# Kernel optimization log

Measured on AMD Instinct MI355X. Metric: run time of the kernel, lower is better.

The kernel has to match this reference:

```python
import jax, jax.numpy as jnp
import numpy as np

B, S, E, H = 4, 1024, 1024, 16
HD = E // H
MAX_SEQ = 5000


def setup_inputs() -> dict:
    key = jax.random.key(0)
    ks = jax.random.split(key, 10)
    def lin(kw, kb):
        w = jax.random.normal(kw, (E, E), dtype=jnp.float32) * (1.0 / np.sqrt(E))
        b = jax.random.normal(kb, (E,), dtype=jnp.float32) * 0.01
        return w, b
    wq, bq = lin(ks[0], ks[1])
    wk, bk = lin(ks[2], ks[3])
    wv, bv = lin(ks[4], ks[5])
    wo, bo = lin(ks[6], ks[7])
    rpe_table = jax.random.normal(ks[8], (H, 2 * MAX_SEQ - 1, HD), dtype=jnp.float32) * 0.02
    x = jax.random.normal(ks[9], (B, S, E), dtype=jnp.float32)
    return {"x": x, "wq": wq, "bq": bq, "wk": wk, "bk": bk,
            "wv": wv, "bv": bv, "wo": wo, "bo": bo, "rpe_table": rpe_table}


def reference(x, wq, bq, wk, bk, wv, bv, wo, bo, rpe_table):
    b, s, e = x.shape
    scale = 1.0 / np.sqrt(HD)
    # projections (torch Linear: y = x @ W^T + b), reshape to (b, h, s, hd)
    q = (x @ wq.T + bq).reshape(b, s, H, HD).transpose(0, 2, 1, 3)
    k = (x @ wk.T + bk).reshape(b, s, H, HD).transpose(0, 2, 1, 3)
    v = (x @ wv.T + bv).reshape(b, s, H, HD).transpose(0, 2, 1, 3)
    scores = jnp.einsum('bhqd,bhkd->bhqk', q, k) * scale
    # RPE: rpe[h, q, k, d] = table[h, q - k + s - 1, d]; factor the einsum:
    # rel[b,h,q,r] = sum_d q[b,h,q,d] * table[h,r,d], then gather r = q - k + s - 1
    table = rpe_table[:, : 2 * s - 1]               # (H, 2s-1, HD)
    rel = jnp.einsum('bhqd,hrd->bhqr', q, table)    # (b, H, s, 2s-1)
    idx = jnp.arange(s)[:, None] - jnp.arange(s)[None, :] + (s - 1)  # (s, s)
    rpe_scores = jnp.take_along_axis(
        rel, jnp.broadcast_to(idx[None, None], (b, H, s, s)), axis=-1)
    attn = jax.nn.softmax(scores + rpe_scores, axis=-1)
    ctx = jnp.einsum('bhqk,bhkd->bhqd', attn, v)
    ctx = ctx.transpose(0, 2, 1, 3).reshape(b, s, e)
    return ctx @ wo.T + bo
```

## Files before the change

### kernel.cpp

```cpp
#include <hip/hip_runtime.h>
#include <hip/hip_bf16.h>
#include <stdint.h>

typedef __attribute__((ext_vector_type(8))) short s8v;
typedef __attribute__((ext_vector_type(4))) float f32x4;
typedef __attribute__((ext_vector_type(16))) float f32x16;

union V16 { uint4 u4; unsigned int u[4]; s8v s; };

__device__ inline s8v u4_to_s8(uint4 v) { V16 c; c.u4 = v; return c.s; }
__device__ inline s8v words_to_s8(unsigned int a, unsigned int b, unsigned int c, unsigned int d) {
  V16 t; t.u[0] = a; t.u[1] = b; t.u[2] = c; t.u[3] = d; return t.s;
}
__device__ inline unsigned short f2b(float f) {
  __hip_bfloat16 h = __float2bfloat16(f);
  unsigned short u; __builtin_memcpy(&u, &h, 2); return u;
}
__device__ inline unsigned int pack2(float lo, float hi) {
  return ((unsigned int)f2b(hi) << 16) | (unsigned int)f2b(lo);
}
__device__ inline unsigned int cvtpk(float lo, float hi) {
  unsigned int r; asm("v_cvt_pk_bf16_f32 %0, %1, %2" : "=v"(r) : "v"(lo), "v"(hi)); return r;
}
__device__ inline float exp2_fast(float x) {
#if __has_builtin(__builtin_amdgcn_exp2f)
  return __builtin_amdgcn_exp2f(x);
#else
  float y; asm("v_exp_f32 %0, %1" : "=v"(y) : "v"(x)); return y;
#endif
}
__device__ inline void gld16(const void* g, void* lds) {
  __builtin_amdgcn_global_load_lds((const __attribute__((address_space(1))) void*)g,
                                   (__attribute__((address_space(3))) void*)lds, 16, 0, 0);
}

#define LOG2E 1.4426950408889634f

__global__ void cvt_all_kernel(const float* __restrict__ x, const float* __restrict__ wq,
                               const float* __restrict__ wk, const float* __restrict__ wv,
                               const float* __restrict__ wo,
                               __hip_bfloat16* __restrict__ XB, __hip_bfloat16* __restrict__ WQKV,
                               __hip_bfloat16* __restrict__ WOb) {
  size_t i = ((size_t)blockIdx.x * 256 + threadIdx.x) * 8;
  const float* src; __hip_bfloat16* dst; size_t off;
  if (i < 4194304)      { src = x;  dst = XB;             off = i; }
  else if (i < 5242880) { src = wq; dst = WQKV;           off = i - 4194304; }
  else if (i < 6291456) { src = wk; dst = WQKV + 1048576; off = i - 5242880; }
  else if (i < 7340032) { src = wv; dst = WQKV + 2097152; off = i - 6291456; }
  else                  { src = wo; dst = WOb;            off = i - 7340032; }
  const float4* s4 = (const float4*)(src + off);
  float4 a = s4[0], b = s4[1];
  uint4 o;
  o.x = pack2(a.x, a.y); o.y = pack2(a.z, a.w);
  o.z = pack2(b.x, b.y); o.w = pack2(b.z, b.w);
  *(uint4*)(dst + off) = o;
}

__global__ void cvt_tbl_kernel(const float* __restrict__ tb, __hip_bfloat16* __restrict__ TBL) {
  size_t i = ((size_t)blockIdx.x * 256 + threadIdx.x) * 8;
  int h = (int)(i >> 17);
  int rem = (int)(i & 131071);
  int r = rem >> 6, c = rem & 63;
  uint4 o;
  if (r < 2047) {
    const float4* s4 = (const float4*)(tb + ((size_t)h * 9999 + r) * 64 + c);
    float4 a = s4[0], b = s4[1];
    o.x = pack2(a.x * LOG2E, a.y * LOG2E); o.y = pack2(a.z * LOG2E, a.w * LOG2E);
    o.z = pack2(b.x * LOG2E, b.y * LOG2E); o.w = pack2(b.z * LOG2E, b.w * LOG2E);
  } else { o.x = 0u; o.y = 0u; o.z = 0u; o.w = 0u; }
  *(uint4*)(TBL + i) = o;
}

template<int MODE>
__global__ __launch_bounds__(256, 3) void gemm_bt(
    const __hip_bfloat16* __restrict__ A,
    const __hip_bfloat16* __restrict__ Bt,
    const float* __restrict__ bias0,
    const float* __restrict__ bias1,
    void* __restrict__ out0,
    void* __restrict__ out1) {
  __shared__ __align__(16) char smem[32768];
  char* As = smem;
  char* Bs = smem + 16384;
  const int tid = threadIdx.x;
  const int w = tid >> 6, l = tid & 63;
  const int wr = w >> 1, wc = w & 1;
  const int lr = l & 15, lg = l >> 4;
  const int m0 = blockIdx.y * 128, n0 = blockIdx.x * 128;

  f32x4 acc[4][4] = {};

  for (int kt = 0; kt < 16; ++kt) {
    __syncthreads();
    #pragma unroll
    for (int i = 0; i < 4; ++i) {
      const int off = i * 4096 + w * 1024;
      const int loff = off + l * 16;
      const int row = loff >> 7;
      const int cb = loff & 127;
      const int sc = cb ^ ((row & 7) << 4);
      gld16((const char*)A  + (size_t)(m0 + row) * 2048 + kt * 128 + sc, As + off);
      gld16((const char*)Bt + (size_t)(n0 + row) * 2048 + kt * 128 + sc, Bs + off);
    }
    asm volatile("s_waitcnt vmcnt(0)" ::: "memory");
    __syncthreads();
    #pragma unroll
    for (int ks = 0; ks < 2; ++ks) {
      uint4 af[4], bf4[4];
      #pragma unroll
      for (int i = 0; i < 4; ++i) {
        const int ra = wr * 64 + i * 16 + lr;
        const int rb = wc * 64 + i * 16 + lr;
        const int cb = ks * 64 + lg * 16;
        af[i]  = *(const uint4*)(As + ra * 128 + (cb ^ ((ra & 7) << 4)));
        bf4[i] = *(const uint4*)(Bs + rb * 128 + (cb ^ ((rb & 7) << 4)));
      }
      #pragma unroll
      for (int i = 0; i < 4; ++i) {
        #pragma unroll
        for (int j = 0; j < 4; ++j)
          acc[i][j] = __builtin_amdgcn_mfma_f32_16x16x32_bf16(u4_to_s8(af[i]), u4_to_s8(bf4[j]), acc[i][j], 0, 0, 0);
      }
    }
  }

  const int mrow = m0 + wr * 64 + lg * 4;
  const int ncol = n0 + wc * 64 + lr;

  if constexpr (MODE == 0) {
    const float KSCALE = 0.125f * LOG2E;
    #pragma unroll
    for (int j = 0; j < 4; ++j) {
      const int n = ncol + j * 16;
      const bool isQ = n < 1024;
      __hip_bfloat16* op = isQ ? (__hip_bfloat16*)out0 : (__hip_bfloat16*)out1;
      const int nn = isQ ? n : n - 1024;
      const float bia = isQ ? bias0[n] : bias1[n - 1024];
      const float sc = isQ ? 1.0f : KSCALE;
      const int hh = nn >> 6, hd = nn & 63;
      #pragma unroll
      for (int i = 0; i < 4; ++i) {
        #pragma unroll
        for (int r = 0; r < 4; ++r) {
          const int m = mrow + i * 16 + r;
          const int bb = m >> 10, ss = m & 1023;
          op[(((size_t)(bb * 16 + hh)) * 1024 + ss) * 64 + hd] = __float2bfloat16((acc[i][j][r] + bia) * sc);
        }
      }
    }
  } else if constexpr (MODE == 1) {
    #pragma unroll
    for (int i = 0; i < 4; ++i) {
      #pragma unroll
      for (int r = 0; r < 4; ++r) {
        const int f = mrow + i * 16 + r;
        const float bia = bias0[f];
        const int fh = f >> 6, fd = f & 63;
        #pragma unroll
        for (int j = 0; j < 4; ++j) {
          const int bs = ncol + j * 16;
          const int bb = bs >> 10, ss = bs & 1023;
          ((__hip_bfloat16*)out0)[(size_t)bb * 1048576 + (size_t)fh * 65536 + fd * 1024 + ss] =
              __float2bfloat16(acc[i][j][r] + bia);
        }
      }
    }
  } else {
    #pragma unroll
    for (int j = 0; j < 4; ++j) {
      const int n = ncol + j * 16;
      const float bia = bias0[n];
      #pragma unroll
      for (int i = 0; i < 4; ++i) {
        #pragma unroll
        for (int r = 0; r < 4; ++r) {
          const int m = mrow + i * 16 + r;
          ((float*)out0)[(size_t)m * 1024 + n] = acc[i][j][r] + bia;
        }
      }
    }
  }
}

__global__ __launch_bounds__(256, 2) void attn_kernel(
    const __hip_bfloat16* __restrict__ Qg,
    const __hip_bfloat16* __restrict__ Kg,
    const __hip_bfloat16* __restrict__ VTg,
    const __hip_bfloat16* __restrict__ Tg,
    __hip_bfloat16* __restrict__ Cg) {
  __shared__ __align__(16) char smem[73984];
  char* Klds = smem;
  char* Vlds = smem + 8192;
  char* Tlds = smem + 16384;
  const int tid = threadIdx.x;
  const int w = tid >> 6, l = tid & 63;
  const int ql = l & 31, half = l >> 5;
  char* relw = smem + 40960 + w * 8192;
  char* dumpp = smem + 73728 + l * 4;

  const int bx = blockIdx.x;
  const int qt = bx & 7, h = (bx >> 3) & 15, b = bx >> 7;
  const int qb = qt * 128;
  const int q0 = qb + 32 * w;

  const size_t bh = (size_t)(b * 16 + h);
  const char* Qb = (const char*)Qg + bh * 131072;
  const char* Kb = (const char*)Kg + bh * 131072;
  const char* Vb = (const char*)VTg + bh * 131072;
  const char* Tb = (const char*)Tg + (size_t)h * 262144;

  const int relsw = ql * 256 + ((ql & 15) << 4);
  const int u4 = (ql << 2) - (half << 4);
  const int qlh = ql - 4 * half;
  const int k0sw = ql * 128 + ((ql & 7) << 4);
  const int k1sw = (32 + ql) * 128 + ((ql & 7) << 4);

  s8v qv[4];
  {
    const char* qrow = Qb + (size_t)(q0 + ql) * 128 + half * 16;
    #pragma unroll
    for (int ds = 0; ds < 4; ++ds) qv[ds] = u4_to_s8(*(const uint4*)(qrow + ds * 32));
  }

  f32x16 cacc0 = {}, cacc1 = {};
  float mL = -1.0e30f, lsum = 0.0f;

  int rbase = qb + 960;

  for (int kt = 0; kt < 16; ++kt, rbase -= 64) {
    const int k0 = kt * 64;
    __syncthreads();
    #pragma unroll
    for (int i = 0; i < 2; ++i) {
      const int off = i * 4096 + w * 1024;
      const int loff = off + l * 16;
      const int row = loff >> 7, cb = loff & 127;
      const int sc = cb ^ ((row & 7) << 4);
      gld16(Kb + (size_t)(k0 + row) * 128 + sc, Klds + off);
      gld16(Vb + (size_t)row * 2048 + (size_t)k0 * 2 + sc, Vlds + off);
    }
    {
      const unsigned cb0 = (unsigned)(rbase >> 6);
      const int nstage = (kt == 0) ? 3 : 1;
      for (int j = 0; j < nstage; ++j) {
        const int slot = (int)((cb0 + (unsigned)j) % 3u);
        const char* src = Tb + (size_t)(rbase + 64 * j) * 128;
        char* dst = Tlds + slot * 8192;
        #pragma unroll
        for (int i = 0; i < 2; ++i) {
          const int off = i * 4096 + w * 1024;
          const int loff = off + l * 16;
          const int row = loff >> 7, cb = loff & 127;
          const int sc = cb ^ ((row & 7) << 4);
          gld16(src + (size_t)row * 128 + sc, dst + off);
        }
      }
    }
    asm volatile("s_waitcnt vmcnt(0)" ::: "memory");
    __syncthreads();

    __builtin_amdgcn_s_setprio(1);
    f32x16 p0 = {}, p1 = {};
    #pragma unroll
    for (int ds = 0; ds < 4; ++ds) {
      const int cb = ds * 32 + half * 16;
      uint4 kf0 = *(const uint4*)(Klds + (k0sw ^ cb));
      uint4 kf1 = *(const uint4*)(Klds + (k1sw ^ cb));
      p0 = __builtin_amdgcn_mfma_f32_32x32x16_bf16(u4_to_s8(kf0), qv[ds], p0, 0, 0, 0);
      p1 = __builtin_amdgcn_mfma_f32_32x32x16_bf16(u4_to_s8(kf1), qv[ds], p1, 0, 0, 0);
    }
    #pragma unroll
    for (int t = 0; t < 3; ++t) {
      const int slot = (int)(((unsigned)(rbase >> 6) + (unsigned)((w + t) >> 1)) % 3u);
      const int rowin = ((w + t) & 1) * 32 + ql;
      const int tbsw = slot * 8192 + rowin * 128 + ((ql & 7) << 4);
      f32x16 racc = {};
      #pragma unroll
      for (int ds = 0; ds < 4; ++ds) {
        const int cb = ds * 32 + half * 16;
        uint4 tf = *(const uint4*)(Tlds + (tbsw ^ cb));
        racc = __builtin_amdgcn_mfma_f32_32x32x16_bf16(u4_to_s8(tf), qv[ds], racc, 0, 0, 0);
      }
      #pragma unroll
      for (int g = 0; g < 4; ++g) {
        #pragma unroll
        for (int j = 0; j < 4; ++j) {
          const int C4 = 4 * (63 - 32 * t - j - 8 * g);
          char* dst = relw + (relsw ^ ((u4 + C4) & 252));
          if (t == 2) dst = (j + 8 * g < qlh) ? dst : dumpp;
          *(float*)dst = racc[4 * g + j];
        }
      }
    }
    __builtin_amdgcn_s_setprio(0);

    #pragma unroll
    for (int mp = 0; mp < 4; ++mp) {
      const int X0 = 32 * mp + 16 * half;
      f32x4 r0 = *(const f32x4*)(relw + (relsw ^ X0));
      f32x4 r1 = *(const f32x4*)(relw + (relsw ^ (X0 + 128)));
      #pragma unroll
      for (int j = 0; j < 4; ++j) {
        p0[4 * mp + j] += r0[j];
        p1[4 * mp + j] += r1[j];
      }
    }

    float pmax = p0[0];
    #pragma unroll
    for (int r = 1; r < 16; ++r) pmax = fmaxf(pmax, p0[r]);
    #pragma unroll
    for (int r = 0; r < 16; ++r) pmax = fmaxf(pmax, p1[r]);
    pmax = fmaxf(pmax, __shfl_xor(pmax, 32));
    if (!__all(pmax - mL <= 12.0f)) {
      const float mnew = fmaxf(mL, pmax);
      const float corr = exp2_fast(mL - mnew);
      mL = mnew;
      lsum *= corr;
      #pragma unroll
      for (int r = 0; r < 16; ++r) {
        const float cr = __shfl(corr, (r & 3) + 8 * (r >> 2) + 4 * half);
        cacc0[r] *= cr;
        cacc1[r] *= cr;
      }
    }
    float psum = 0.0f;
    #pragma unroll
    for (int r = 0; r < 16; ++r) {
      p0[r] = exp2_fast(p0[r] - mL);
      p1[r] = exp2_fast(p1[r] - mL);
      psum += p0[r] + p1[r];
    }
    psum += __shfl_xor(psum, 32);
    lsum += psum;

    unsigned int w0[8], w1[8];
    #pragma unroll
    for (int jw = 0; jw < 8; ++jw) {
      w0[jw] = cvtpk(p0[2 * jw], p0[2 * jw + 1]);
      w1[jw] = cvtpk(p1[2 * jw], p1[2 * jw + 1]);
    }
    unsigned int r0x[4], r1x[4];
    #pragma unroll
    for (int i = 0; i < 4; ++i) {
      const int jkeep = (i & 1) + 4 * (i >> 1);
      const int jsend = jkeep + 2;
      unsigned int v0 = half ? w0[jkeep] : w0[jsend];
      unsigned int v1 = half ? w1[jkeep] : w1[jsend];
      r0x[i] = (unsigned int)__shfl_xor((int)v0, 32);
      r1x[i] = (unsigned int)__shfl_xor((int)v1, 32);
    }
    __builtin_amdgcn_s_setprio(1);
    #pragma unroll
    for (int ks = 0; ks < 4; ++ks) {
      const int mm = ks & 1;
      unsigned int f0_, f1_, f2_, f3_;
      if (ks < 2) {
        f0_ = half ? r0x[2 * mm]     : w0[4 * mm];
        f1_ = half ? r0x[2 * mm + 1] : w0[4 * mm + 1];
        f2_ = half ? w0[4 * mm + 2]  : r0x[2 * mm];
        f3_ = half ? w0[4 * mm + 3]  : r0x[2 * mm + 1];
      } else {
        f0_ = half ? r1x[2 * mm]     : w1[4 * mm];
        f1_ = half ? r1x[2 * mm + 1] : w1[4 * mm + 1];
        f2_ = half ? w1[4 * mm + 2]  : r1x[2 * mm];
        f3_ = half ? w1[4 * mm + 3]  : r1x[2 * mm + 1];
      }
      s8v pf = words_to_s8(f0_, f1_, f2_, f3_);
      const int cb = ks * 32 + half * 16;
      uint4 vf0 = *(const uint4*)(Vlds + (k0sw ^ cb));
      uint4 vf1 = *(const uint4*)(Vlds + (k1sw ^ cb));
      cacc0 = __builtin_amdgcn_mfma_f32_32x32x16_bf16(pf, u4_to_s8(vf0), cacc0, 0, 0, 0);
      cacc1 = __builtin_amdgcn_mfma_f32_32x32x16_bf16(pf, u4_to_s8(vf1), cacc1, 0, 0, 0);
    }
    __builtin_amdgcn_s_setprio(0);
  }

  #pragma unroll
  for (int r = 0; r < 16; ++r) {
    const int qr = (r & 3) + 8 * (r >> 2) + 4 * half;
    const float inv = 1.0f / __shfl(lsum, qr);
    const size_t row = (size_t)b * 1024 + q0 + qr;
    const size_t basei = row * 1024 + h * 64 + ql;
    Cg[basei]      = __float2bfloat16(cacc0[r] * inv);
    Cg[basei + 32] = __float2bfloat16(cacc1[r] * inv);
  }
}

extern "C" void kernel_launch(void* const* d_in, const int* in_sizes, int n_in,
                              void* d_out, int out_size, void* d_ws, size_t ws_size,
                              hipStream_t stream) {
  (void)in_sizes; (void)n_in; (void)out_size; (void)ws_size;
  const float* x  = (const float*)d_in[0];
  const float* wq = (const float*)d_in[1];
  const float* bq = (const float*)d_in[2];
  const float* wk = (const float*)d_in[3];
  const float* bk = (const float*)d_in[4];
  const float* wv = (const float*)d_in[5];
  const float* bv = (const float*)d_in[6];
  const float* wo = (const float*)d_in[7];
  const float* bo = (const float*)d_in[8];
  const float* tb = (const float*)d_in[9];

  char* ws = (char*)d_ws;
  __hip_bfloat16* XB   = (__hip_bfloat16*)(ws);
  __hip_bfloat16* WQKV = (__hip_bfloat16*)(ws + 8388608);
  __hip_bfloat16* WOb  = (__hip_bfloat16*)(ws + 14680064);
  __hip_bfloat16* TBL  = (__hip_bfloat16*)(ws + 16777216);
  __hip_bfloat16* QB   = (__hip_bfloat16*)(ws + 20971520);
  __hip_bfloat16* KB   = (__hip_bfloat16*)(ws + 29360128);
  __hip_bfloat16* VTB  = (__hip_bfloat16*)(ws + 37748736);
  __hip_bfloat16* CTX  = (__hip_bfloat16*)(ws + 46137344);

  cvt_all_kernel<<<4096, 256, 0, stream>>>(x, wq, wk, wv, wo, XB, WQKV, WOb);
  cvt_tbl_kernel<<<1024, 256, 0, stream>>>(tb, TBL);
  gemm_bt<0><<<dim3(16, 32), 256, 0, stream>>>(XB, WQKV, bq, bk, (void*)QB, (void*)KB);
  gemm_bt<1><<<dim3(32, 8), 256, 0, stream>>>(WQKV + 2097152, XB, bv, nullptr, (void*)VTB, nullptr);
  attn_kernel<<<512, 256, 0, stream>>>(QB, KB, VTB, TBL, CTX);
  gemm_bt<2><<<dim3(8, 32), 256, 0, stream>>>(CTX, WOb, bo, nullptr, d_out, nullptr);
}
```

Before: 123.9 us.

## Fuse conversion kernels, merge QKV GEMMs, and software-pipeline attention loads

The two fp32-to-bf16 conversion kernels become one launch. The Q/K and V projection GEMMs merge into a single 24x32 grid, with V written transposed using vectorised 4-element stores. The attention kernel now issues the next tile's K, V and RPE-table loads after each stage's compute, with partial vmcnt waits and barriers replacing the full drain. Its block-to-work mapping is remapped, and the max/sum reductions become trees. Together these cut launch overhead and hide global-load latency, at the cost of more barriers and fragile vmcnt accounting.

```diff
diff --git a/kernel.cpp b/kernel.cpp
--- a/kernel.cpp
+++ b/kernel.cpp
@@ -36,49 +36,48 @@
 
 #define LOG2E 1.4426950408889634f
 
-__global__ void cvt_all_kernel(const float* __restrict__ x, const float* __restrict__ wq,
-                               const float* __restrict__ wk, const float* __restrict__ wv,
-                               const float* __restrict__ wo,
-                               __hip_bfloat16* __restrict__ XB, __hip_bfloat16* __restrict__ WQKV,
-                               __hip_bfloat16* __restrict__ WOb) {
-  size_t i = ((size_t)blockIdx.x * 256 + threadIdx.x) * 8;
-  const float* src; __hip_bfloat16* dst; size_t off;
-  if (i < 4194304)      { src = x;  dst = XB;             off = i; }
-  else if (i < 5242880) { src = wq; dst = WQKV;           off = i - 4194304; }
-  else if (i < 6291456) { src = wk; dst = WQKV + 1048576; off = i - 5242880; }
-  else if (i < 7340032) { src = wv; dst = WQKV + 2097152; off = i - 6291456; }
-  else                  { src = wo; dst = WOb;            off = i - 7340032; }
-  const float4* s4 = (const float4*)(src + off);
-  float4 a = s4[0], b = s4[1];
-  uint4 o;
-  o.x = pack2(a.x, a.y); o.y = pack2(a.z, a.w);
-  o.z = pack2(b.x, b.y); o.w = pack2(b.z, b.w);
-  *(uint4*)(dst + off) = o;
-}
-
-__global__ void cvt_tbl_kernel(const float* __restrict__ tb, __hip_bfloat16* __restrict__ TBL) {
-  size_t i = ((size_t)blockIdx.x * 256 + threadIdx.x) * 8;
-  int h = (int)(i >> 17);
-  int rem = (int)(i & 131071);
-  int r = rem >> 6, c = rem & 63;
-  uint4 o;
-  if (r < 2047) {
-    const float4* s4 = (const float4*)(tb + ((size_t)h * 9999 + r) * 64 + c);
+__global__ void cvt_fused_kernel(const float* __restrict__ x, const float* __restrict__ wq,
+                                 const float* __restrict__ wk, const float* __restrict__ wv,
+                                 const float* __restrict__ wo, const float* __restrict__ tb,
+                                 __hip_bfloat16* __restrict__ XB, __hip_bfloat16* __restrict__ WQKV,
+                                 __hip_bfloat16* __restrict__ WOb, __hip_bfloat16* __restrict__ TBL) {
+  const int bid = blockIdx.x;
+  if (bid < 4096) {
+    size_t i = ((size_t)bid * 256 + threadIdx.x) * 8;
+    const float* src; __hip_bfloat16* dst; size_t off;
+    if (i < 4194304)      { src = x;  dst = XB;             off = i; }
+    else if (i < 5242880) { src = wq; dst = WQKV;           off = i - 4194304; }
+    else if (i < 6291456) { src = wk; dst = WQKV + 1048576; off = i - 5242880; }
+    else if (i < 7340032) { src = wv; dst = WQKV + 2097152; off = i - 6291456; }
+    else                  { src = wo; dst = WOb;            off = i - 7340032; }
+    const float4* s4 = (const float4*)(src + off);
     float4 a = s4[0], b = s4[1];
-    o.x = pack2(a.x * LOG2E, a.y * LOG2E); o.y = pack2(a.z * LOG2E, a.w * LOG2E);
-    o.z = pack2(b.x * LOG2E, b.y * LOG2E); o.w = pack2(b.z * LOG2E, b.w * LOG2E);
-  } else { o.x = 0u; o.y = 0u; o.z = 0u; o.w = 0u; }
-  *(uint4*)(TBL + i) = o;
-}
-
-template<int MODE>
-__global__ __launch_bounds__(256, 3) void gemm_bt(
+    uint4 o;
+    o.x = pack2(a.x, a.y); o.y = pack2(a.z, a.w);
+    o.z = pack2(b.x, b.y); o.w = pack2(b.z, b.w);
+    *(uint4*)(dst + off) = o;
+  } else {
+    size_t i = ((size_t)(bid - 4096) * 256 + threadIdx.x) * 8;
+    int h = (int)(i >> 17);
+    int rem = (int)(i & 131071);
+    int r = rem >> 6, c = rem & 63;
+    uint4 o;
+    if (r < 2047) {
+      const float4* s4 = (const float4*)(tb + ((size_t)h * 9999 + r) * 64 + c);
+      float4 a = s4[0], b = s4[1];
+      o.x = pack2(a.x * LOG2E, a.y * LOG2E); o.y = pack2(a.z * LOG2E, a.w * LOG2E);
+      o.z = pack2(b.x * LOG2E, b.y * LOG2E); o.w = pack2(b.z * LOG2E, b.w * LOG2E);
+    } else { o.x = 0u; o.y = 0u; o.z = 0u; o.w = 0u; }
+    *(uint4*)(TBL + i) = o;
+  }
+}
+
+__global__ __launch_bounds__(256, 3) void gemm_qkv(
     const __hip_bfloat16* __restrict__ A,
     const __hip_bfloat16* __restrict__ Bt,
-    const float* __restrict__ bias0,
-    const float* __restrict__ bias1,
-    void* __restrict__ out0,
-    void* __restrict__ out1) {
+    const float* __restrict__ bq, const float* __restrict__ bk, const float* __restrict__ bv,
+    __hip_bfloat16* __restrict__ QB, __hip_bfloat16* __restrict__ KB,
+    __hip_bfloat16* __restrict__ VTB) {
   __shared__ __align__(16) char smem[32768];
   char* As = smem;
   char* Bs = smem + 16384;
@@ -126,18 +125,17 @@
 
   const int mrow = m0 + wr * 64 + lg * 4;
   const int ncol = n0 + wc * 64 + lr;
-
-  if constexpr (MODE == 0) {
-    const float KSCALE = 0.125f * LOG2E;
+  const int cls = blockIdx.x >> 3;
+
+  if (cls < 2) {
+    const float sc = cls ? 0.125f * LOG2E : 1.0f;
+    const float* bias = cls ? bk : bq;
+    __hip_bfloat16* op = cls ? KB : QB;
     #pragma unroll
     for (int j = 0; j < 4; ++j) {
-      const int n = ncol + j * 16;
-      const bool isQ = n < 1024;
-      __hip_bfloat16* op = isQ ? (__hip_bfloat16*)out0 : (__hip_bfloat16*)out1;
-      const int nn = isQ ? n : n - 1024;
-      const float bia = isQ ? bias0[n] : bias1[n - 1024];
-      const float sc = isQ ? 1.0f : KSCALE;
-      const int hh = nn >> 6, hd = nn & 63;
+      const int n = ncol - cls * 1024 + j * 16;
+      const float bia = bias[n];
+      const int hh = n >> 6, hd = n & 63;
       #pragma unroll
       for (int i = 0; i < 4; ++i) {
         #pragma unroll
@@ -148,35 +146,87 @@
         }
       }
     }
-  } else if constexpr (MODE == 1) {
+  } else {
+    #pragma unroll
+    for (int j = 0; j < 4; ++j) {
+      const int f = ncol - 2048 + j * 16;
+      const float bia = bv[f];
+      const int fh = f >> 6, fd = f & 63;
+      #pragma unroll
+      for (int i = 0; i < 4; ++i) {
+        const int m = mrow + i * 16;
+        const int bb = m >> 10, ss = m & 1023;
+        ushort4 qv;
+        qv.x = f2b(acc[i][j][0] + bia); qv.y = f2b(acc[i][j][1] + bia);
+        qv.z = f2b(acc[i][j][2] + bia); qv.w = f2b(acc[i][j][3] + bia);
+        *(ushort4*)((char*)VTB + (((size_t)bb * 1048576 + (size_t)fh * 65536 + fd * 1024 + ss) * 2)) = qv;
+      }
+    }
+  }
+}
+
+__global__ __launch_bounds__(256, 3) void gemm_out(
+    const __hip_bfloat16* __restrict__ A,
+    const __hip_bfloat16* __restrict__ Bt,
+    const float* __restrict__ bo,
+    float* __restrict__ out) {
+  __shared__ __align__(16) char smem[32768];
+  char* As = smem;
+  char* Bs = smem + 16384;
+  const int tid = threadIdx.x;
+  const int w = tid >> 6, l = tid & 63;
+  const int wr = w >> 1, wc = w & 1;
+  const int lr = l & 15, lg = l >> 4;
+  const int m0 = blockIdx.y * 128, n0 = blockIdx.x * 128;
+
+  f32x4 acc[4][4] = {};
+
+  for (int kt = 0; kt < 16; ++kt) {
+    __syncthreads();
     #pragma unroll
     for (int i = 0; i < 4; ++i) {
-      #pragma unroll
-      for (int r = 0; r < 4; ++r) {
-        const int f = mrow + i * 16 + r;
-        const float bia = bias0[f];
-        const int fh = f >> 6, fd = f & 63;
-        #pragma unroll
-        for (int j = 0; j < 4; ++j) {
-          const int bs = ncol + j * 16;
-          const int bb = bs >> 10, ss = bs & 1023;
-          ((__hip_bfloat16*)out0)[(size_t)bb * 1048576 + (size_t)fh * 65536 + fd * 1024 + ss] =
-              __float2bfloat16(acc[i][j][r] + bia);
-        }
-      }
-    }
-  } else {
-    #pragma unroll
-    for (int j = 0; j < 4; ++j) {
-      const int n = ncol + j * 16;
-      const float bia = bias0[n];
+      const int off = i * 4096 + w * 1024;
+      const int loff = off + l * 16;
+      const int row = loff >> 7;
+      const int cb = loff & 127;
+      const int sc = cb ^ ((row & 7) << 4);
+      gld16((const char*)A  + (size_t)(m0 + row) * 2048 + kt * 128 + sc, As + off);
+      gld16((const char*)Bt + (size_t)(n0 + row) * 2048 + kt * 128 + sc, Bs + off);
+    }
+    asm volatile("s_waitcnt vmcnt(0)" ::: "memory");
+    __syncthreads();
+    #pragma unroll
+    for (int ks = 0; ks < 2; ++ks) {
+      uint4 af[4], bf4[4];
+      #pragma unroll
+      for (int i = 0; i < 4; ++i) {
+        const int ra = wr * 64 + i * 16 + lr;
+        const int rb = wc * 64 + i * 16 + lr;
+        const int cb = ks * 64 + lg * 16;
+        af[i]  = *(const uint4*)(As + ra * 128 + (cb ^ ((ra & 7) << 4)));
+        bf4[i] = *(const uint4*)(Bs + rb * 128 + (cb ^ ((rb & 7) << 4)));
+      }
       #pragma unroll
       for (int i = 0; i < 4; ++i) {
         #pragma unroll
-        for (int r = 0; r < 4; ++r) {
-          const int m = mrow + i * 16 + r;
-          ((float*)out0)[(size_t)m * 1024 + n] = acc[i][j][r] + bia;
-        }
+        for (int j = 0; j < 4; ++j)
+          acc[i][j] = __builtin_amdgcn_mfma_f32_16x16x32_bf16(u4_to_s8(af[i]), u4_to_s8(bf4[j]), acc[i][j], 0, 0, 0);
+      }
+    }
+  }
+
+  const int mrow = m0 + wr * 64 + lg * 4;
+  const int ncol = n0 + wc * 64 + lr;
+  #pragma unroll
+  for (int j = 0; j < 4; ++j) {
+    const int n = ncol + j * 16;
+    const float bia = bo[n];
+    #pragma unroll
+    for (int i = 0; i < 4; ++i) {
+      #pragma unroll
+      for (int r = 0; r < 4; ++r) {
+        const int m = mrow + i * 16 + r;
+        out[(size_t)m * 1024 + n] = acc[i][j][r] + bia;
       }
     }
   }
@@ -199,7 +249,9 @@
   char* dumpp = smem + 73728 + l * 4;
 
   const int bx = blockIdx.x;
-  const int qt = bx & 7, h = (bx >> 3) & 15, b = bx >> 7;
+  const int work = (bx & 7) * 64 + (bx >> 3);
+  const int b = work & 3, hqt = work >> 2;
+  const int h = hqt >> 3, qt = hqt & 7;
   const int qb = qt * 128;
   const int q0 = qb + 32 * w;
 
@@ -215,52 +267,62 @@
   const int k0sw = ql * 128 + ((ql & 7) << 4);
   const int k1sw = (32 + ql) * 128 + ((ql & 7) << 4);
 
-  s8v qv[4];
-  {
-    const char* qrow = Qb + (size_t)(q0 + ql) * 128 + half * 16;
-    #pragma unroll
-    for (int ds = 0; ds < 4; ++ds) qv[ds] = u4_to_s8(*(const uint4*)(qrow + ds * 32));
-  }
-
-  f32x16 cacc0 = {}, cacc1 = {};
-  float mL = -1.0e30f, lsum = 0.0f;
-
-  int rbase = qb + 960;
-
-  for (int kt = 0; kt < 16; ++kt, rbase -= 64) {
-    const int k0 = kt * 64;
-    __syncthreads();
+  auto stageK = [&](int k0n) {
     #pragma unroll
     for (int i = 0; i < 2; ++i) {
       const int off = i * 4096 + w * 1024;
       const int loff = off + l * 16;
       const int row = loff >> 7, cb = loff & 127;
       const int sc = cb ^ ((row & 7) << 4);
-      gld16(Kb + (size_t)(k0 + row) * 128 + sc, Klds + off);
-      gld16(Vb + (size_t)row * 2048 + (size_t)k0 * 2 + sc, Vlds + off);
-    }
-    {
-      const unsigned cb0 = (unsigned)(rbase >> 6);
-      const int nstage = (kt == 0) ? 3 : 1;
-      for (int j = 0; j < nstage; ++j) {
-        const int slot = (int)((cb0 + (unsigned)j) % 3u);
-        const char* src = Tb + (size_t)(rbase + 64 * j) * 128;
-        char* dst = Tlds + slot * 8192;
-        #pragma unroll
-        for (int i = 0; i < 2; ++i) {
-          const int off = i * 4096 + w * 1024;
-          const int loff = off + l * 16;
-          const int row = loff >> 7, cb = loff & 127;
-          const int sc = cb ^ ((row & 7) << 4);
-          gld16(src + (size_t)row * 128 + sc, dst + off);
-        }
-      }
-    }
-    asm volatile("s_waitcnt vmcnt(0)" ::: "memory");
-    __syncthreads();
-
+      gld16(Kb + (size_t)(k0n + row) * 128 + sc, Klds + off);
+    }
+  };
+  auto stageV = [&](int k0n) {
+    #pragma unroll
+    for (int i = 0; i < 2; ++i) {
+      const int off = i * 4096 + w * 1024;
+      const int loff = off + l * 16;
+      const int row = loff >> 7, cb = loff & 127;
+      const int sc = cb ^ ((row & 7) << 4);
+      gld16(Vb + (size_t)row * 2048 + (size_t)k0n * 2 + sc, Vlds + off);
+    }
+  };
+  auto stageT = [&](int rbn) {
+    const int slot = (int)(((unsigned)(rbn >> 6)) % 3u);
+    char* dst = Tlds + slot * 8192;
+    #pragma unroll
+    for (int i = 0; i < 2; ++i) {
+      const int off = i * 4096 + w * 1024;
+      const int loff = off + l * 16;
+      const int row = loff >> 7, cb = loff & 127;
+      const int sc = cb ^ ((row & 7) << 4);
+      gld16(Tb + (size_t)(rbn + row) * 128 + sc, dst + off);
+    }
+  };
+
+  s8v qv[4];
+  {
+    const char* qrow = Qb + (size_t)(q0 + ql) * 128 + half * 16;
+    #pragma unroll
+    for (int ds = 0; ds < 4; ++ds) qv[ds] = u4_to_s8(*(const uint4*)(qrow + ds * 32));
+  }
+
+  f32x16 cacc0 = {}, cacc1 = {};
+  float mL = -1.0e30f, lsum = 0.0f;
+
+  int rbase = qb + 960;
+
+  stageK(0);
+  stageT(rbase); stageT(rbase + 64); stageT(rbase + 128);
+  stageV(0);
+
+  for (int kt = 0; kt < 16; ++kt, rbase -= 64) {
+    if (kt == 0) { asm volatile("s_waitcnt vmcnt(8)" ::: "memory"); }
+    else         { asm volatile("s_waitcnt vmcnt(4)" ::: "memory"); }
+    __builtin_amdgcn_s_barrier();
+
+    f32x16 p0 = {}, p1 = {};
     __builtin_amdgcn_s_setprio(1);
-    f32x16 p0 = {}, p1 = {};
     #pragma unroll
     for (int ds = 0; ds < 4; ++ds) {
       const int cb = ds * 32 + half * 16;
@@ -269,6 +331,15 @@
       p0 = __builtin_amdgcn_mfma_f32_32x32x16_bf16(u4_to_s8(kf0), qv[ds], p0, 0, 0, 0);
       p1 = __builtin_amdgcn_mfma_f32_32x32x16_bf16(u4_to_s8(kf1), qv[ds], p1, 0, 0, 0);
     }
+    __builtin_amdgcn_s_setprio(0);
+
+    __builtin_amdgcn_s_barrier();
+    stageK(((kt + 1) & 15) * 64);
+
+    asm volatile("s_waitcnt vmcnt(4)" ::: "memory");
+    __builtin_amdgcn_s_barrier();
+
+    __builtin_amdgcn_s_setprio(1);
     #pragma unroll
     for (int t = 0; t < 3; ++t) {
       const int slot = (int)(((unsigned)(rbase >> 6) + (unsigned)((w + t) >> 1)) % 3u);
@@ -294,6 +365,9 @@
     }
     __builtin_amdgcn_s_setprio(0);
 
+    __builtin_amdgcn_s_barrier();
+    { int rbn = rbase - 64; if (rbn < 0) rbn = 0; stageT(rbn); }
+
     #pragma unroll
     for (int mp = 0; mp < 4; ++mp) {
       const int X0 = 32 * mp + 16 * half;
@@ -306,11 +380,12 @@
       }
     }
 
-    float pmax = p0[0];
-    #pragma unroll
-    for (int r = 1; r < 16; ++r) pmax = fmaxf(pmax, p0[r]);
-    #pragma unroll
-    for (int r = 0; r < 16; ++r) pmax = fmaxf(pmax, p1[r]);
+    float mx[8];
+    #pragma unroll
+    for (int i = 0; i < 8; ++i)
+      mx[i] = fmaxf(fmaxf(p0[2 * i], p0[2 * i + 1]), fmaxf(p1[2 * i], p1[2 * i + 1]));
+    float pmax = fmaxf(fmaxf(fmaxf(mx[0], mx[1]), fmaxf(mx[2], mx[3])),
+                       fmaxf(fmaxf(mx[4], mx[5]), fmaxf(mx[6], mx[7])));
     pmax = fmaxf(pmax, __shfl_xor(pmax, 32));
     if (!__all(pmax - mL <= 12.0f)) {
       const float mnew = fmaxf(mL, pmax);
@@ -324,13 +399,16 @@
         cacc1[r] *= cr;
       }
     }
-    float psum = 0.0f;
     #pragma unroll
     for (int r = 0; r < 16; ++r) {
       p0[r] = exp2_fast(p0[r] - mL);
       p1[r] = exp2_fast(p1[r] - mL);
-      psum += p0[r] + p1[r];
-    }
+    }
+    float sm[8];
+    #pragma unroll
+    for (int i = 0; i < 8; ++i)
+      sm[i] = (p0[2 * i] + p0[2 * i + 1]) + (p1[2 * i] + p1[2 * i + 1]);
+    float psum = ((sm[0] + sm[1]) + (sm[2] + sm[3])) + ((sm[4] + sm[5]) + (sm[6] + sm[7]));
     psum += __shfl_xor(psum, 32);
     lsum += psum;
 
@@ -350,6 +428,10 @@
       r0x[i] = (unsigned int)__shfl_xor((int)v0, 32);
       r1x[i] = (unsigned int)__shfl_xor((int)v1, 32);
     }
+
+    asm volatile("s_waitcnt vmcnt(4)" ::: "memory");
+    __builtin_amdgcn_s_barrier();
+
     __builtin_amdgcn_s_setprio(1);
     #pragma unroll
     for (int ks = 0; ks < 4; ++ks) {
@@ -374,7 +456,11 @@
       cacc1 = __builtin_amdgcn_mfma_f32_32x32x16_bf16(pf, u4_to_s8(vf1), cacc1, 0, 0, 0);
     }
     __builtin_amdgcn_s_setprio(0);
-  }
+
+    __builtin_amdgcn_s_barrier();
+    stageV(((kt + 1) & 15) * 64);
+  }
+  asm volatile("s_waitcnt vmcnt(0)" ::: "memory");
 
   #pragma unroll
   for (int r = 0; r < 16; ++r) {
@@ -412,10 +498,8 @@
   __hip_bfloat16* VTB  = (__hip_bfloat16*)(ws + 37748736);
   __hip_bfloat16* CTX  = (__hip_bfloat16*)(ws + 46137344);
 
-  cvt_all_kernel<<<4096, 256, 0, stream>>>(x, wq, wk, wv, wo, XB, WQKV, WOb);
-  cvt_tbl_kernel<<<1024, 256, 0, stream>>>(tb, TBL);
-  gemm_bt<0><<<dim3(16, 32), 256, 0, stream>>>(XB, WQKV, bq, bk, (void*)QB, (void*)KB);
-  gemm_bt<1><<<dim3(32, 8), 256, 0, stream>>>(WQKV + 2097152, XB, bv, nullptr, (void*)VTB, nullptr);
+  cvt_fused_kernel<<<5120, 256, 0, stream>>>(x, wq, wk, wv, wo, tb, XB, WQKV, WOb, TBL);
+  gemm_qkv<<<dim3(24, 32), 256, 0, stream>>>(XB, WQKV, bq, bk, bv, QB, KB, VTB);
   attn_kernel<<<512, 256, 0, stream>>>(QB, KB, VTB, TBL, CTX);
-  gemm_bt<2><<<dim3(8, 32), 256, 0, stream>>>(CTX, WOb, bo, nullptr, d_out, nullptr);
-}
+  gemm_out<<<dim3(8, 32), 256, 0, stream>>>(CTX, WOb, bo, (float*)d_out);
+}
```

Result: faster. 113.9 us (-8.1%).
